# Performance work log

Measured on AMD Instinct MI355X. Metric: run time of the kernel, lower is better.

The kernel has to match this reference:

```python
import jax, jax.numpy as jnp
import numpy as np

N, E, DEG, DIM, NFP, NSEQ = 8192, 65536, 16, 64, 10000, 1024
LGNN, RAD, LOUT, NCLS = 3, 2, 2, 2


def setup_inputs() -> dict:
    key = jax.random.key(0)
    ks = jax.random.split(key, 24)
    s = 0.02
    return {
        "fingerprints": jax.random.randint(ks[0], (N,), 0, NFP + 1),
        "atom_degree_list": jax.random.randint(ks[1], (N, DEG), 0, N),
        "bond_feature": jax.random.normal(ks[2], (E, 10), jnp.float32),
        "bond_degree_list": jax.random.randint(ks[3], (N, DEG), 0, E),
        "i_bond_j": jax.random.randint(ks[4], (E, 2), 0, N),
        # scale down so adjacency @ hs does not saturate the sigmoids
        "adjacency": jax.random.uniform(ks[5], (N, N), jnp.float32) * (1.0 / 128.0),
        "words": jax.random.normal(ks[6], (NSEQ,), jnp.float32),
        "embed_table": jax.random.normal(ks[7], (NFP + 1, DIM), jnp.float32) * s,
        "bond_W": jax.random.normal(ks[8], (10, DIM), jnp.float32) * s,
        "bond_b": jnp.zeros((DIM,), jnp.float32),
        "sub_W": jax.random.normal(ks[9], (RAD, DIM, DIM), jnp.float32) * s,
        "sub_b": jnp.zeros((RAD, DIM), jnp.float32),
        "neigh_W": jax.random.normal(ks[10], (LGNN, 2 * DIM, DIM), jnp.float32) * s,
        "neigh_b": jnp.zeros((LGNN, DIM), jnp.float32),
        "side_W": jax.random.normal(ks[11], (LGNN, DIM, DIM), jnp.float32) * s,
        "side_b": jnp.zeros((LGNN, DIM), jnp.float32),
        "fc_W": jax.random.uniform(ks[12], (NSEQ, DIM), jnp.float32, -0.01, 0.01),
        "fc_b": jnp.zeros((DIM,), jnp.float32),
        "out_W": jax.random.normal(ks[13], (LOUT, 2 * DIM, 2 * DIM), jnp.float32) * s,
        "out_b": jnp.zeros((LOUT, 2 * DIM), jnp.float32),
        "inter_W": jax.random.normal(ks[14], (2 * DIM, NCLS), jnp.float32) * s,
        "inter_b": jnp.zeros((NCLS,), jnp.float32),
    }


def reference(fingerprints, atom_degree_list, bond_feature, bond_degree_list,
              i_bond_j, adjacency, words, embed_table, bond_W, bond_b,
              sub_W, sub_b, neigh_W, neigh_b, side_W, side_b,
              fc_W, fc_b, out_W, out_b, inter_W, inter_b):
    # sub_graph: residual dense-adjacency propagation
    x = embed_table[fingerprints]                       # [N, dim]
    for i in range(RAD):
        hs = jax.nn.relu(x @ sub_W[i] + sub_b[i])
        x = x + adjacency @ hs

    # gnn: gather neighbors, concat, linear+leaky_relu, sum, sigmoid updates
    bond_f = bond_feature @ bond_W + bond_b             # [E, dim]
    atom_f = x
    for i in range(LGNN):
        bn = bond_f[bond_degree_list]                   # [N, DEG, dim]
        an = atom_f[atom_degree_list]                   # [N, DEG, dim]
        nf = jnp.concatenate([an, bn], axis=-1)         # [N, DEG, 2*dim]
        nf = jax.nn.leaky_relu(nf @ neigh_W[i] + neigh_b[i], 0.01)
        atom_f = jax.nn.sigmoid(atom_f + nf.sum(axis=-2))
        pair = atom_f[i_bond_j].sum(axis=-2)            # [E, dim]
        bond_f = jax.nn.sigmoid(bond_f + pair @ side_W[i] + side_b[i])

    disease_vector = jnp.mean(x + atom_f, axis=0)[None, :]   # [1, dim]

    # miRNA vector via MLP
    mirna_vector = words.reshape(1, -1) @ fc_W + fc_b        # [1, dim]

    cat = jnp.concatenate([disease_vector, mirna_vector], axis=1)  # [1, 2*dim]
    for j in range(LOUT):
        cat = jax.nn.relu(cat @ out_W[j] + out_b[j])
    association = cat @ inter_W + inter_b                    # [1, n_classes]
    return association
```

## Files before the change

### kernel.cpp

```cpp
#include <hip/hip_runtime.h>
#include <hip/hip_bf16.h>
#include <cstdint>
#include <cstddef>

#define N_ATOM 8192
#define N_EDGE 65536
#define DEG    16
#define DIM    64
#define ADJ_S  4
#define BM     64
#define BK     64

typedef __attribute__((ext_vector_type(8))) short bf16x8_t;
typedef __attribute__((ext_vector_type(4))) float f32x4_t;

__device__ __forceinline__ float sigmoidf_(float z) {
  return 1.0f / (1.0f + __expf(-z));
}
__device__ __forceinline__ float lrelu_(float z) {
  return z > 0.0f ? z : 0.01f * z;
}
__device__ __forceinline__ unsigned short f2bfu(float f) {
  union { __hip_bfloat16 h; unsigned short u; } v;
  v.h = __float2bfloat16(f);
  return v.u;
}
__device__ __forceinline__ float bf2f(unsigned short u) {
  union { unsigned int i; float f; } v;
  v.i = ((unsigned int)u) << 16;
  return v.f;
}
__device__ __forceinline__ float4 cvt4f(ushort4 u) {
  return make_float4(bf2f(u.x), bf2f(u.y), bf2f(u.z), bf2f(u.w));
}
__device__ __forceinline__ ushort4 cvt4b(float4 f) {
  ushort4 u;
  u.x = f2bfu(f.x); u.y = f2bfu(f.y); u.z = f2bfu(f.z); u.w = f2bfu(f.w);
  return u;
}
__device__ __forceinline__ bf16x8_t cvt8(const float4 a, const float4 b) {
  bf16x8_t r;
  r[0] = (short)f2bfu(a.x); r[1] = (short)f2bfu(a.y);
  r[2] = (short)f2bfu(a.z); r[3] = (short)f2bfu(a.w);
  r[4] = (short)f2bfu(b.x); r[5] = (short)f2bfu(b.y);
  r[6] = (short)f2bfu(b.z); r[7] = (short)f2bfu(b.w);
  return r;
}
__device__ __forceinline__ void gload16(const void* g, void* l) {
  __builtin_amdgcn_global_load_lds(
      (const __attribute__((address_space(1))) void*)g,
      (__attribute__((address_space(3))) void*)l, 16, 0, 0);
}

__global__ __launch_bounds__(256) void k_front(
    const int* __restrict__ fp, const float* __restrict__ emb,
    float* __restrict__ x, const float* __restrict__ W,
    const float* __restrict__ b, unsigned short* __restrict__ hsT,
    const float* __restrict__ bfeat, const float* __restrict__ bW,
    const float* __restrict__ bb, unsigned short* __restrict__ bond_bf,
    const float* __restrict__ Wbn0, unsigned short* __restrict__ B_bf,
    const float* __restrict__ words, const float* __restrict__ fcW,
    float* __restrict__ mp2) {
  __shared__ float ps[64][68];
  __shared__ float Ws[64][64];
  const int t = threadIdx.x;
  const int r = t >> 4, dq = t & 15, d0 = dq * 4;
  if (blockIdx.x < (N_ATOM / 16)) {
    const int row = blockIdx.x * 16 + r;
    float4 v = reinterpret_cast<const float4*>(emb)[(size_t)fp[row] * 16 + dq];
    reinterpret_cast<float4*>(x)[(size_t)row * 16 + dq] = v;
    *reinterpret_cast<float4*>(&ps[r][d0]) = v;
#pragma unroll
    for (int q = 0; q < 4; ++q) {
      int p = t + q * 256;
      reinterpret_cast<float4*>(&Ws[0][0])[p] =
          reinterpret_cast<const float4*>(W)[p];
    }
    __syncthreads();
    float4 acc = reinterpret_cast<const float4*>(b)[dq];
#pragma unroll
    for (int k = 0; k < 64; ++k) {
      float xv = ps[r][k];
      float4 wv = *reinterpret_cast<const float4*>(&Ws[k][d0]);
      acc.x = fmaf(xv, wv.x, acc.x);
      acc.y = fmaf(xv, wv.y, acc.y);
      acc.z = fmaf(xv, wv.z, acc.z);
      acc.w = fmaf(xv, wv.w, acc.w);
    }
    float a4[4] = {acc.x, acc.y, acc.z, acc.w};
#pragma unroll
    for (int j = 0; j < 4; ++j)
      hsT[(size_t)(d0 + j) * N_ATOM + row] = f2bfu(fmaxf(a4[j], 0.0f));
  } else if (blockIdx.x < (N_ATOM / 16 + N_EDGE / 64)) {
    const int row0 = (blockIdx.x - N_ATOM / 16) * 64;
    float4 acc[4];
#pragma unroll
    for (int g = 0; g < 4; ++g) acc[g] = reinterpret_cast<const float4*>(bb)[dq];
#pragma unroll
    for (int k = 0; k < 10; ++k) {
      float4 wv = reinterpret_cast<const float4*>(bW)[k * 16 + dq];
#pragma unroll
      for (int g = 0; g < 4; ++g) {
        float xv = bfeat[(size_t)(row0 + g * 16 + r) * 10 + k];
        acc[g].x = fmaf(xv, wv.x, acc[g].x);
        acc[g].y = fmaf(xv, wv.y, acc[g].y);
        acc[g].z = fmaf(xv, wv.z, acc[g].z);
        acc[g].w = fmaf(xv, wv.w, acc[g].w);
      }
    }
#pragma unroll
    for (int g = 0; g < 4; ++g) {
      int row = row0 + g * 16 + r;
      reinterpret_cast<ushort4*>(bond_bf)[(size_t)row * 16 + dq] = cvt4b(acc[g]);
      *reinterpret_cast<float4*>(&ps[g * 16 + r][d0]) = acc[g];
    }
#pragma unroll
    for (int q = 0; q < 4; ++q) {
      int p = t + q * 256;
      reinterpret_cast<float4*>(&Ws[0][0])[p] =
          reinterpret_cast<const float4*>(Wbn0)[p];
    }
    __syncthreads();
    float4 a2[4];
#pragma unroll
    for (int g = 0; g < 4; ++g) a2[g] = make_float4(0.f, 0.f, 0.f, 0.f);
    for (int k = 0; k < 64; ++k) {
      float4 wv = *reinterpret_cast<const float4*>(&Ws[k][d0]);
#pragma unroll
      for (int g = 0; g < 4; ++g) {
        float xv = ps[g * 16 + r][k];
        a2[g].x = fmaf(xv, wv.x, a2[g].x);
        a2[g].y = fmaf(xv, wv.y, a2[g].y);
        a2[g].z = fmaf(xv, wv.z, a2[g].z);
        a2[g].w = fmaf(xv, wv.w, a2[g].w);
      }
    }
#pragma unroll
    for (int g = 0; g < 4; ++g) {
      int row = row0 + g * 16 + r;
      reinterpret_cast<ushort4*>(B_bf)[(size_t)row * 16 + dq] = cvt4b(a2[g]);
    }
  } else {
    const int mb = blockIdx.x - (N_ATOM / 16 + N_EDGE / 64);
    const int k = mb * 16 + r;
    float wv = words[k];
    float4 fv = reinterpret_cast<const float4*>(fcW)[(size_t)k * 16 + dq];
    float4 acc = make_float4(wv * fv.x, wv * fv.y, wv * fv.z, wv * fv.w);
    float4* red4 = reinterpret_cast<float4*>(&Ws[0][0]);
    red4[t] = acc;
    __syncthreads();
    for (int h = 8; h >= 1; h >>= 1) {
      if (r < h) {
        float4 o = red4[t + h * 16];
        acc.x += o.x; acc.y += o.y; acc.z += o.z; acc.w += o.w;
        red4[t] = acc;
      }
      __syncthreads();
    }
    if (r == 0) reinterpret_cast<float4*>(mp2)[mb * 16 + dq] = acc;
  }
}

__global__ __launch_bounds__(256) void k_red_hs(
    const float* __restrict__ part, float* __restrict__ x,
    const float* __restrict__ W, const float* __restrict__ b,
    unsigned short* __restrict__ hsT) {
  __shared__ float xs[16][68];
  __shared__ float Ws[64][64];
  const int t = threadIdx.x;
  const int r = t >> 4, dq = t & 15, d0 = dq * 4;
  const int row = blockIdx.x * 16 + r;
  float4 v = reinterpret_cast<const float4*>(x)[(size_t)row * 16 + dq];
#pragma unroll
  for (int s = 0; s < ADJ_S; ++s) {
    float4 p = reinterpret_cast<const float4*>(part)
                   [(size_t)s * (N_ATOM * 16) + (size_t)row * 16 + dq];
    v.x += p.x; v.y += p.y; v.z += p.z; v.w += p.w;
  }
  reinterpret_cast<float4*>(x)[(size_t)row * 16 + dq] = v;
  *reinterpret_cast<float4*>(&xs[r][d0]) = v;
#pragma unroll
  for (int q = 0; q < 4; ++q) {
    int p = t + q * 256;
    reinterpret_cast<float4*>(&Ws[0][0])[p] =
        reinterpret_cast<const float4*>(W)[p];
  }
  __syncthreads();
  float4 acc = reinterpret_cast<const float4*>(b)[dq];
#pragma unroll
  for (int k = 0; k < 64; ++k) {
    float xv = xs[r][k];
    float4 wv = *reinterpret_cast<const float4*>(&Ws[k][d0]);
    acc.x = fmaf(xv, wv.x, acc.x);
    acc.y = fmaf(xv, wv.y, acc.y);
    acc.z = fmaf(xv, wv.z, acc.z);
    acc.w = fmaf(xv, wv.w, acc.w);
  }
  float a4[4] = {acc.x, acc.y, acc.z, acc.w};
#pragma unroll
  for (int j = 0; j < 4; ++j)
    hsT[(size_t)(d0 + j) * N_ATOM + row] = f2bfu(fmaxf(a4[j], 0.0f));
}

__global__ __launch_bounds__(256) void k_adjmm(
    const float* __restrict__ adj, const unsigned short* __restrict__ hsT,
    float* __restrict__ part) {
  __shared__ float          Abuf[2][BM * BK];
  __shared__ unsigned short Bbuf[2][64 * BK];
  const int t = threadIdx.x;
  const int lane = t & 63, w = t >> 6;
  const int lr = lane & 15, lg = lane >> 4;
  const int row0 = blockIdx.x * BM;
  const int kbase = blockIdx.y * (N_ATOM / ADJ_S);
  const int NSTEP = (N_ATOM / ADJ_S) / BK;

  size_t aSrc[4]; int aLds[4];
#pragma unroll
  for (int j = 0; j < 4; ++j) {
    int c = j * 256 + t;
    int row = c >> 4, u = c & 15;
    int us = (u & 8) | ((u & 7) ^ (row & 7));
    aSrc[j] = (size_t)(row0 + row) * N_ATOM + kbase + us * 4;
    aLds[j] = j * 1024 + w * 256;
  }
  size_t bSrc[2]; int bLds[2];
#pragma unroll
  for (int j = 0; j < 2; ++j) {
    int c = j * 256 + t;
    int row = c >> 3, u = c & 7;
    int us = u ^ (row & 7);
    bSrc[j] = (size_t)row * N_ATOM + kbase + us * 8;
    bLds[j] = j * 2048 + w * 512;
  }

  f32x4_t acc[4];
#pragma unroll
  for (int n = 0; n < 4; ++n) acc[n] = (f32x4_t){0.f, 0.f, 0.f, 0.f};

#define STAGE(buf, kt)                                                        \
  {                                                                           \
    _Pragma("unroll")                                                         \
    for (int j = 0; j < 4; ++j)                                               \
      gload16(adj + aSrc[j] + (kt) * BK, &Abuf[buf][aLds[j]]);                \
    _Pragma("unroll")                                                         \
    for (int j = 0; j < 2; ++j)                                               \
      gload16(hsT + bSrc[j] + (kt) * BK, &Bbuf[buf][bLds[j]]);                \
  }

  STAGE(0, 0);
  int cur = 0;
  const int Rl = w * 16 + lr;
  for (int kt = 0; kt < NSTEP; ++kt) {
    if (kt + 1 < NSTEP) {
      STAGE(cur ^ 1, kt + 1);
      asm volatile("s_waitcnt vmcnt(6)" ::: "memory");
    } else {
      asm volatile("s_waitcnt vmcnt(0)" ::: "memory");
    }
    __builtin_amdgcn_s_barrier();
    __builtin_amdgcn_sched_barrier(0);
#pragma unroll
    for (int kf = 0; kf < 2; ++kf) {
      int ua = kf * 8 + ((2 * lg) ^ (Rl & 7));
      int ub = kf * 8 + ((2 * lg + 1) ^ (Rl & 7));
      float4 fa = *reinterpret_cast<const float4*>(&Abuf[cur][Rl * 64 + ua * 4]);
      float4 fb = *reinterpret_cast<const float4*>(&Abuf[cur][Rl * 64 + ub * 4]);
      bf16x8_t a = cvt8(fa, fb);
#pragma unroll
      for (int n = 0; n < 4; ++n) {
        int Rb = n * 16 + lr;
        int us = (kf * 4 + lg) ^ (Rb & 7);
        bf16x8_t bv = *reinterpret_cast<const bf16x8_t*>(&Bbuf[cur][Rb * 64 + us * 8]);
        acc[n] = __builtin_amdgcn_mfma_f32_16x16x32_bf16(a, bv, acc[n], 0, 0, 0);
      }
    }
    __builtin_amdgcn_sched_barrier(0);
    __builtin_amdgcn_s_barrier();
    cur ^= 1;
  }
#undef STAGE

  float* pp = part + (size_t)blockIdx.y * (N_ATOM * DIM);
#pragma unroll
  for (int n = 0; n < 4; ++n)
#pragma unroll
    for (int rg = 0; rg < 4; ++rg) {
      int row = row0 + w * 16 + lg * 4 + rg;
      int col = n * 16 + lr;
      pp[(size_t)row * DIM + col] = acc[n][rg];
    }
}

__global__ __launch_bounds__(256) void k_A0(
    float* __restrict__ atom_f, const float* __restrict__ nW0,
    const float* __restrict__ nb0, unsigned short* __restrict__ A,
    const float* __restrict__ part, float* __restrict__ x) {
  __shared__ float xs[16][68];
  __shared__ float Ws[64][64];
  int t = threadIdx.x;
  int r = t >> 4, dq = t & 15, d0 = dq * 4;
  int row = blockIdx.x * 16 + r;
  float4 v = reinterpret_cast<const float4*>(x)[(size_t)row * 16 + dq];
#pragma unroll
  for (int s = 0; s < ADJ_S; ++s) {
    float4 p = reinterpret_cast<const float4*>(part)
                   [(size_t)s * (N_ATOM * 16) + (size_t)row * 16 + dq];
    v.x += p.x; v.y += p.y; v.z += p.z; v.w += p.w;
  }
  reinterpret_cast<float4*>(x)[(size_t)row * 16 + dq] = v;
  reinterpret_cast<float4*>(atom_f)[(size_t)row * 16 + dq] = v;
  *reinterpret_cast<float4*>(&xs[r][d0]) = v;
#pragma unroll
  for (int q = 0; q < 4; ++q) {
    int p = t + q * 256;
    reinterpret_cast<float4*>(&Ws[0][0])[p] = reinterpret_cast<const float4*>(nW0)[p];
  }
  __syncthreads();
  float4 acc = reinterpret_cast<const float4*>(nb0)[dq];
#pragma unroll
  for (int k = 0; k < 64; ++k) {
    float xv = xs[r][k];
    float4 wv = *reinterpret_cast<const float4*>(&Ws[k][d0]);
    acc.x = fmaf(xv, wv.x, acc.x);
    acc.y = fmaf(xv, wv.y, acc.y);
    acc.z = fmaf(xv, wv.z, acc.z);
    acc.w = fmaf(xv, wv.w, acc.w);
  }
  reinterpret_cast<ushort4*>(A)[(size_t)row * 16 + dq] = cvt4b(acc);
}

__global__ __launch_bounds__(256) void k_upd(
    const int* __restrict__ adl, const int* __restrict__ bdl,
    const unsigned short* __restrict__ A, const unsigned short* __restrict__ B,
    float* __restrict__ atom_f, const float* __restrict__ WanN,
    const float* __restrict__ nbN, unsigned short* __restrict__ A_next,
    const float* __restrict__ x, float* __restrict__ mp, int has_next) {
  __shared__ float xs[16][68];
  __shared__ float Ws[64][64];
  int t = threadIdx.x;
  int r = t >> 4, dq = t & 15, d0 = dq * 4;
  int n = blockIdx.x * 16 + r;
  float4 s = make_float4(0.f, 0.f, 0.f, 0.f);
#pragma unroll
  for (int g = 0; g < DEG; ++g) {
    int ai = adl[n * DEG + g];
    int bi = bdl[n * DEG + g];
    float4 va = cvt4f(reinterpret_cast<const ushort4*>(A)[(size_t)ai * 16 + dq]);
    float4 vb = cvt4f(reinterpret_cast<const ushort4*>(B)[(size_t)bi * 16 + dq]);
    s.x += lrelu_(va.x + vb.x);
    s.y += lrelu_(va.y + vb.y);
    s.z += lrelu_(va.z + vb.z);
    s.w += lrelu_(va.w + vb.w);
  }
  float4 af = reinterpret_cast<const float4*>(atom_f)[(size_t)n * 16 + dq];
  af.x = sigmoidf_(af.x + s.x);
  af.y = sigmoidf_(af.y + s.y);
  af.z = sigmoidf_(af.z + s.z);
  af.w = sigmoidf_(af.w + s.w);
  reinterpret_cast<float4*>(atom_f)[(size_t)n * 16 + dq] = af;
  if (has_next) {
    *reinterpret_cast<float4*>(&xs[r][d0]) = af;
#pragma unroll
    for (int q = 0; q < 4; ++q) {
      int p = t + q * 256;
      reinterpret_cast<float4*>(&Ws[0][0])[p] =
          reinterpret_cast<const float4*>(WanN)[p];
    }
    __syncthreads();
    float4 acc = reinterpret_cast<const float4*>(nbN)[dq];
#pragma unroll
    for (int k = 0; k < 64; ++k) {
      float xv = xs[r][k];
      float4 wv = *reinterpret_cast<const float4*>(&Ws[k][d0]);
      acc.x = fmaf(xv, wv.x, acc.x);
      acc.y = fmaf(xv, wv.y, acc.y);
      acc.z = fmaf(xv, wv.z, acc.z);
      acc.w = fmaf(xv, wv.w, acc.w);
    }
    reinterpret_cast<ushort4*>(A_next)[(size_t)n * 16 + dq] = cvt4b(acc);
  } else {
    float4 xv = reinterpret_cast<const float4*>(x)[(size_t)n * 16 + dq];
    float4 c = make_float4(af.x + xv.x, af.y + xv.y, af.z + xv.z, af.w + xv.w);
    float4* red4 = reinterpret_cast<float4*>(&Ws[0][0]);
    red4[t] = c;
    __syncthreads();
    for (int h = 8; h >= 1; h >>= 1) {
      if (r < h) {
        float4 o = red4[t + h * 16];
        c.x += o.x; c.y += o.y; c.z += o.z; c.w += o.w;
        red4[t] = c;
      }
      __syncthreads();
    }
    if (r == 0) reinterpret_cast<float4*>(mp)[blockIdx.x * 16 + dq] = c;
  }
}

__global__ __launch_bounds__(256) void k_side(
    const int* __restrict__ ibj, const float* __restrict__ atom_f,
    const float* __restrict__ sW, const float* __restrict__ sb,
    unsigned short* __restrict__ bond_bf, const float* __restrict__ WbnN,
    unsigned short* __restrict__ B_next, int write_bond) {
  __shared__ float ps[64][68];
  __shared__ float Ws[64][64];
  int t = threadIdx.x;
  int r = t >> 4, dq = t & 15, d0 = dq * 4;
  int e0 = blockIdx.x * 64;
#pragma unroll
  for (int q = 0; q < 4; ++q) {
    int p = t + q * 256;
    reinterpret_cast<float4*>(&Ws[0][0])[p] = reinterpret_cast<const float4*>(sW)[p];
  }
#pragma unroll
  for (int g = 0; g < 4; ++g) {
    int e = e0 + g * 16 + r;
    int i0 = ibj[e * 2], i1 = ibj[e * 2 + 1];
    float4 p0 = reinterpret_cast<const float4*>(atom_f)[(size_t)i0 * 16 + dq];
    float4 p1 = reinterpret_cast<const float4*>(atom_f)[(size_t)i1 * 16 + dq];
    *reinterpret_cast<float4*>(&ps[g * 16 + r][d0]) =
        make_float4(p0.x + p1.x, p0.y + p1.y, p0.z + p1.z, p0.w + p1.w);
  }
  __syncthreads();
  float4 acc[4];
#pragma unroll
  for (int g = 0; g < 4; ++g) acc[g] = reinterpret_cast<const float4*>(sb)[dq];
  for (int k = 0; k < 64; ++k) {
    float4 wv = *reinterpret_cast<const float4*>(&Ws[k][d0]);
#pragma unroll
    for (int g = 0; g < 4; ++g) {
      float xv = ps[g * 16 + r][k];
      acc[g].x = fmaf(xv, wv.x, acc[g].x);
      acc[g].y = fmaf(xv, wv.y, acc[g].y);
      acc[g].z = fmaf(xv, wv.z, acc[g].z);
      acc[g].w = fmaf(xv, wv.w, acc[g].w);
    }
  }
  float4 bf[4];
#pragma unroll
  for (int g = 0; g < 4; ++g) {
    int e = e0 + g * 16 + r;
    float4 b0 = cvt4f(reinterpret_cast<const ushort4*>(bond_bf)[(size_t)e * 16 + dq]);
    bf[g].x = sigmoidf_(b0.x + acc[g].x);
    bf[g].y = sigmoidf_(b0.y + acc[g].y);
    bf[g].z = sigmoidf_(b0.z + acc[g].z);
    bf[g].w = sigmoidf_(b0.w + acc[g].w);
    if (write_bond)
      reinterpret_cast<ushort4*>(bond_bf)[(size_t)e * 16 + dq] = cvt4b(bf[g]);
  }
  __syncthreads();
#pragma unroll
  for (int g = 0; g < 4; ++g)
    *reinterpret_cast<float4*>(&ps[g * 16 + r][d0]) = bf[g];
#pragma unroll
  for (int q = 0; q < 4; ++q) {
    int p = t + q * 256;
    reinterpret_cast<float4*>(&Ws[0][0])[p] =
        reinterpret_cast<const float4*>(WbnN)[p];
  }
  __syncthreads();
  float4 a2[4];
#pragma unroll
  for (int g = 0; g < 4; ++g) a2[g] = make_float4(0.f, 0.f, 0.f, 0.f);
  for (int k = 0; k < 64; ++k) {
    float4 wv = *reinterpret_cast<const float4*>(&Ws[k][d0]);
#pragma unroll
    for (int g = 0; g < 4; ++g) {
      float xv = ps[g * 16 + r][k];
      a2[g].x = fmaf(xv, wv.x, a2[g].x);
      a2[g].y = fmaf(xv, wv.y, a2[g].y);
      a2[g].z = fmaf(xv, wv.z, a2[g].z);
      a2[g].w = fmaf(xv, wv.w, a2[g].w);
    }
  }
#pragma unroll
  for (int g = 0; g < 4; ++g) {
    int e = e0 + g * 16 + r;
    reinterpret_cast<ushort4*>(B_next)[(size_t)e * 16 + dq] = cvt4b(a2[g]);
  }
}

__global__ __launch_bounds__(256) void k_tail(
    const float* __restrict__ mp, const float* __restrict__ mp2,
    const float* __restrict__ fcb, const float* __restrict__ oW,
    const float* __restrict__ ob, const float* __restrict__ iW,
    const float* __restrict__ ib, float* __restrict__ out) {
  __shared__ float red[4][64];
  __shared__ float red2[4][64];
  __shared__ float cat[128];
  int t = threadIdx.x;
  int col = t & 63, ch = t >> 6;
  {
    float s = 0.f;
    for (int w = ch * 128; w < ch * 128 + 128; ++w) s += mp[w * 64 + col];
    red[ch][col] = s;
    float s2 = 0.f;
    for (int w = ch * 16; w < ch * 16 + 16; ++w) s2 += mp2[w * 64 + col];
    red2[ch][col] = s2;
  }
  __syncthreads();
  if (t < 64) {
    cat[t] = (red[0][t] + red[1][t] + red[2][t] + red[3][t]) * (1.0f / N_ATOM);
  } else if (t < 128) {
    int d = t - 64;
    cat[64 + d] = fcb[d] + red2[0][d] + red2[1][d] + red2[2][d] + red2[3][d];
  }
  __syncthreads();
  for (int j = 0; j < 2; ++j) {
    float s = 0.f;
    if (t < 128) {
      s = ob[j * 128 + t];
      for (int k = 0; k < 128; ++k)
        s = fmaf(cat[k], oW[(size_t)j * 128 * 128 + k * 128 + t], s);
      s = fmaxf(s, 0.f);
    }
    __syncthreads();
    if (t < 128) cat[t] = s;
    __syncthreads();
  }
  if (t < 2) {
    float s = ib[t];
    for (int k = 0; k < 128; ++k) s = fmaf(cat[k], iW[k * 2 + t], s);
    out[t] = s;
  }
}

extern "C" void kernel_launch(void* const* d_in, const int* in_sizes, int n_in,
                              void* d_out, int out_size, void* d_ws, size_t ws_size,
                              hipStream_t stream) {
  const int*   fp    = (const int*)  d_in[0];
  const int*   adl   = (const int*)  d_in[1];
  const float* bfeat = (const float*)d_in[2];
  const int*   bdl   = (const int*)  d_in[3];
  const int*   ibj   = (const int*)  d_in[4];
  const float* adj   = (const float*)d_in[5];
  const float* words = (const float*)d_in[6];
  const float* emb   = (const float*)d_in[7];
  const float* bW    = (const float*)d_in[8];
  const float* bb    = (const float*)d_in[9];
  const float* subW  = (const float*)d_in[10];
  const float* subb  = (const float*)d_in[11];
  const float* nW    = (const float*)d_in[12];
  const float* nb    = (const float*)d_in[13];
  const float* sW    = (const float*)d_in[14];
  const float* sb    = (const float*)d_in[15];
  const float* fcW   = (const float*)d_in[16];
  const float* fcb   = (const float*)d_in[17];
  const float* oW    = (const float*)d_in[18];
  const float* ob    = (const float*)d_in[19];
  const float* iW    = (const float*)d_in[20];
  const float* ib    = (const float*)d_in[21];
  float* out = (float*)d_out;

  char* ws = (char*)d_ws;
  const size_t MB = 1ull << 20;
  float*          x      = (float*)(ws + 0 * MB);
  float*          atom_f = (float*)(ws + 2 * MB);
  unsigned short* A0_bf  = (unsigned short*)(ws + 4 * MB);
  unsigned short* A1_bf  = (unsigned short*)(ws + 5 * MB);
  unsigned short* hsT    = (unsigned short*)(ws + 6 * MB);
  float*          mp     = (float*)(ws + 7 * MB);
  float*          mp2    = (float*)(ws + 7 * MB + 512 * 1024);
  unsigned short* bond_bf= (unsigned short*)(ws + 8 * MB);
  unsigned short* B_bf   = (unsigned short*)(ws + 16 * MB);
  float*          part   = (float*)(ws + 32 * MB);

  dim3 gmm(N_ATOM / BM, ADJ_S);

  k_front<<<N_ATOM / 16 + N_EDGE / 64 + 64, 256, 0, stream>>>(
      fp, emb, x, subW, subb, hsT, bfeat, bW, bb, bond_bf,
      nW + 64 * 64, B_bf, words, fcW, mp2);
  k_adjmm<<<gmm, 256, 0, stream>>>(adj, hsT, part);
  k_red_hs<<<N_ATOM / 16, 256, 0, stream>>>(part, x, subW + 64 * 64,
                                            subb + 64, hsT);
  k_adjmm<<<gmm, 256, 0, stream>>>(adj, hsT, part);

  k_A0<<<N_ATOM / 16, 256, 0, stream>>>(atom_f, nW, nb, A0_bf, part, x);
  k_upd<<<N_ATOM / 16, 256, 0, stream>>>(adl, bdl, A0_bf, B_bf, atom_f,
                                         nW + 1 * 128 * 64, nb + 1 * 64,
                                         A1_bf, x, mp, 1);
  k_side<<<N_EDGE / 64, 256, 0, stream>>>(ibj, atom_f, sW, sb, bond_bf,
                                          nW + 1 * 128 * 64 + 64 * 64, B_bf, 1);
  k_upd<<<N_ATOM / 16, 256, 0, stream>>>(adl, bdl, A1_bf, B_bf, atom_f,
                                         nW + 2 * 128 * 64, nb + 2 * 64,
                                         A0_bf, x, mp, 1);
  k_side<<<N_EDGE / 64, 256, 0, stream>>>(ibj, atom_f, sW + 64 * 64, sb + 64,
                                          bond_bf, nW + 2 * 128 * 64 + 64 * 64,
                                          B_bf, 0);
  k_upd<<<N_ATOM / 16, 256, 0, stream>>>(adl, bdl, A0_bf, B_bf, atom_f,
                                         nullptr, nullptr, nullptr, x, mp, 0);

  k_tail<<<1, 256, 0, stream>>>(mp, mp2, fcb, oW, ob, iW, ib, out);
}
```

Before: 218.0 us.

## Fuse adjacency matmul with reduction and dense epilogue, dropping split-K partials

Replaces the split-K adjacency GEMM (64-row tiles, 4 K-splits writing fp32 partials) and its separate reduce/dense kernels with one kernel per radius step. Each block owns 16 rows and covers the full K range with triple-buffered loads, then applies the residual add and the next 64x64 dense layer in its epilogue. This removes the partial-sum traffic and two launches. In exchange each block reads the whole hsT for only 16 rows, which cuts B reuse fourfold, and the grid becomes 512 blocks with long serial K loops.

```diff
diff --git a/kernel.cpp b/kernel.cpp
--- a/kernel.cpp
+++ b/kernel.cpp
@@ -7,8 +7,6 @@
 #define N_EDGE 65536
 #define DEG    16
 #define DIM    64
-#define ADJ_S  4
-#define BM     64
 #define BK     64
 
 typedef __attribute__((ext_vector_type(8))) short bf16x8_t;
@@ -161,99 +159,54 @@
   }
 }
 
-__global__ __launch_bounds__(256) void k_red_hs(
-    const float* __restrict__ part, float* __restrict__ x,
-    const float* __restrict__ W, const float* __restrict__ b,
-    unsigned short* __restrict__ hsT) {
-  __shared__ float xs[16][68];
-  __shared__ float Ws[64][64];
-  const int t = threadIdx.x;
-  const int r = t >> 4, dq = t & 15, d0 = dq * 4;
-  const int row = blockIdx.x * 16 + r;
-  float4 v = reinterpret_cast<const float4*>(x)[(size_t)row * 16 + dq];
-#pragma unroll
-  for (int s = 0; s < ADJ_S; ++s) {
-    float4 p = reinterpret_cast<const float4*>(part)
-                   [(size_t)s * (N_ATOM * 16) + (size_t)row * 16 + dq];
-    v.x += p.x; v.y += p.y; v.z += p.z; v.w += p.w;
-  }
-  reinterpret_cast<float4*>(x)[(size_t)row * 16 + dq] = v;
-  *reinterpret_cast<float4*>(&xs[r][d0]) = v;
-#pragma unroll
-  for (int q = 0; q < 4; ++q) {
-    int p = t + q * 256;
-    reinterpret_cast<float4*>(&Ws[0][0])[p] =
-        reinterpret_cast<const float4*>(W)[p];
-  }
-  __syncthreads();
-  float4 acc = reinterpret_cast<const float4*>(b)[dq];
-#pragma unroll
-  for (int k = 0; k < 64; ++k) {
-    float xv = xs[r][k];
-    float4 wv = *reinterpret_cast<const float4*>(&Ws[k][d0]);
-    acc.x = fmaf(xv, wv.x, acc.x);
-    acc.y = fmaf(xv, wv.y, acc.y);
-    acc.z = fmaf(xv, wv.z, acc.z);
-    acc.w = fmaf(xv, wv.w, acc.w);
-  }
-  float a4[4] = {acc.x, acc.y, acc.z, acc.w};
-#pragma unroll
-  for (int j = 0; j < 4; ++j)
-    hsT[(size_t)(d0 + j) * N_ATOM + row] = f2bfu(fmaxf(a4[j], 0.0f));
-}
-
-__global__ __launch_bounds__(256) void k_adjmm(
-    const float* __restrict__ adj, const unsigned short* __restrict__ hsT,
-    float* __restrict__ part) {
-  __shared__ float          Abuf[2][BM * BK];
-  __shared__ unsigned short Bbuf[2][64 * BK];
+__global__ __launch_bounds__(256) void k_adjfused(
+    const float* __restrict__ adj, const unsigned short* __restrict__ hsIn,
+    float* __restrict__ x, float* __restrict__ atom_f,
+    const float* __restrict__ Wn, const float* __restrict__ bn,
+    unsigned short* __restrict__ hsOut, unsigned short* __restrict__ A0,
+    int mode) {
+  __shared__ float          Abuf[3][16 * BK];
+  __shared__ unsigned short Bbuf[3][64 * BK];
   const int t = threadIdx.x;
   const int lane = t & 63, w = t >> 6;
   const int lr = lane & 15, lg = lane >> 4;
-  const int row0 = blockIdx.x * BM;
-  const int kbase = blockIdx.y * (N_ATOM / ADJ_S);
-  const int NSTEP = (N_ATOM / ADJ_S) / BK;
-
-  size_t aSrc[4]; int aLds[4];
-#pragma unroll
-  for (int j = 0; j < 4; ++j) {
-    int c = j * 256 + t;
-    int row = c >> 4, u = c & 15;
-    int us = (u & 8) | ((u & 7) ^ (row & 7));
-    aSrc[j] = (size_t)(row0 + row) * N_ATOM + kbase + us * 4;
-    aLds[j] = j * 1024 + w * 256;
-  }
+  const int row0 = blockIdx.x * 16;
+  const int NSTEP = N_ATOM / BK;
+
+  const int arow = t >> 4, au = t & 15;
+  const int aus = (au & 8) | ((au & 7) ^ (arow & 7));
+  const size_t aSrc = (size_t)(row0 + arow) * N_ATOM + aus * 4;
+  const int aLds = w * 256;
   size_t bSrc[2]; int bLds[2];
 #pragma unroll
   for (int j = 0; j < 2; ++j) {
     int c = j * 256 + t;
-    int row = c >> 3, u = c & 7;
-    int us = u ^ (row & 7);
-    bSrc[j] = (size_t)row * N_ATOM + kbase + us * 8;
+    int brow = c >> 3, bu = c & 7;
+    int bus = bu ^ (brow & 7);
+    bSrc[j] = (size_t)brow * N_ATOM + bus * 8;
     bLds[j] = j * 2048 + w * 512;
   }
 
-  f32x4_t acc[4];
-#pragma unroll
-  for (int n = 0; n < 4; ++n) acc[n] = (f32x4_t){0.f, 0.f, 0.f, 0.f};
+  f32x4_t acc = (f32x4_t){0.f, 0.f, 0.f, 0.f};
 
 #define STAGE(buf, kt)                                                        \
   {                                                                           \
-    _Pragma("unroll")                                                         \
-    for (int j = 0; j < 4; ++j)                                               \
-      gload16(adj + aSrc[j] + (kt) * BK, &Abuf[buf][aLds[j]]);                \
+    gload16(adj + aSrc + (size_t)(kt) * BK, &Abuf[buf][aLds]);                \
     _Pragma("unroll")                                                         \
     for (int j = 0; j < 2; ++j)                                               \
-      gload16(hsT + bSrc[j] + (kt) * BK, &Bbuf[buf][bLds[j]]);                \
+      gload16(hsIn + bSrc[j] + (size_t)(kt) * BK, &Bbuf[buf][bLds[j]]);       \
   }
 
   STAGE(0, 0);
+  STAGE(1, 1);
   int cur = 0;
-  const int Rl = w * 16 + lr;
   for (int kt = 0; kt < NSTEP; ++kt) {
-    if (kt + 1 < NSTEP) {
-      STAGE(cur ^ 1, kt + 1);
+    if (kt + 2 < NSTEP) {
+      int nb = cur + 2; if (nb >= 3) nb -= 3;
+      STAGE(nb, kt + 2);
       asm volatile("s_waitcnt vmcnt(6)" ::: "memory");
+    } else if (kt + 1 < NSTEP) {
+      asm volatile("s_waitcnt vmcnt(3)" ::: "memory");
     } else {
       asm volatile("s_waitcnt vmcnt(0)" ::: "memory");
     }
@@ -261,72 +214,65 @@
     __builtin_amdgcn_sched_barrier(0);
 #pragma unroll
     for (int kf = 0; kf < 2; ++kf) {
-      int ua = kf * 8 + ((2 * lg) ^ (Rl & 7));
-      int ub = kf * 8 + ((2 * lg + 1) ^ (Rl & 7));
-      float4 fa = *reinterpret_cast<const float4*>(&Abuf[cur][Rl * 64 + ua * 4]);
-      float4 fb = *reinterpret_cast<const float4*>(&Abuf[cur][Rl * 64 + ub * 4]);
+      int ua = kf * 8 + ((2 * lg) ^ (lr & 7));
+      int ub = kf * 8 + ((2 * lg + 1) ^ (lr & 7));
+      float4 fa = *reinterpret_cast<const float4*>(&Abuf[cur][lr * 64 + ua * 4]);
+      float4 fb = *reinterpret_cast<const float4*>(&Abuf[cur][lr * 64 + ub * 4]);
       bf16x8_t a = cvt8(fa, fb);
-#pragma unroll
-      for (int n = 0; n < 4; ++n) {
-        int Rb = n * 16 + lr;
-        int us = (kf * 4 + lg) ^ (Rb & 7);
-        bf16x8_t bv = *reinterpret_cast<const bf16x8_t*>(&Bbuf[cur][Rb * 64 + us * 8]);
-        acc[n] = __builtin_amdgcn_mfma_f32_16x16x32_bf16(a, bv, acc[n], 0, 0, 0);
-      }
+      int Rb = w * 16 + lr;
+      int us = (kf * 4 + lg) ^ (Rb & 7);
+      bf16x8_t bv = *reinterpret_cast<const bf16x8_t*>(&Bbuf[cur][Rb * 64 + us * 8]);
+      acc = __builtin_amdgcn_mfma_f32_16x16x32_bf16(a, bv, acc, 0, 0, 0);
     }
     __builtin_amdgcn_sched_barrier(0);
     __builtin_amdgcn_s_barrier();
-    cur ^= 1;
+    cur = cur + 1; if (cur >= 3) cur = 0;
   }
 #undef STAGE
 
-  float* pp = part + (size_t)blockIdx.y * (N_ATOM * DIM);
-#pragma unroll
-  for (int n = 0; n < 4; ++n)
-#pragma unroll
-    for (int rg = 0; rg < 4; ++rg) {
-      int row = row0 + w * 16 + lg * 4 + rg;
-      int col = n * 16 + lr;
-      pp[(size_t)row * DIM + col] = acc[n][rg];
-    }
-}
-
-__global__ __launch_bounds__(256) void k_A0(
-    float* __restrict__ atom_f, const float* __restrict__ nW0,
-    const float* __restrict__ nb0, unsigned short* __restrict__ A,
-    const float* __restrict__ part, float* __restrict__ x) {
-  __shared__ float xs[16][68];
-  __shared__ float Ws[64][64];
-  int t = threadIdx.x;
-  int r = t >> 4, dq = t & 15, d0 = dq * 4;
-  int row = blockIdx.x * 16 + r;
-  float4 v = reinterpret_cast<const float4*>(x)[(size_t)row * 16 + dq];
-#pragma unroll
-  for (int s = 0; s < ADJ_S; ++s) {
-    float4 p = reinterpret_cast<const float4*>(part)
-                   [(size_t)s * (N_ATOM * 16) + (size_t)row * 16 + dq];
-    v.x += p.x; v.y += p.y; v.z += p.z; v.w += p.w;
-  }
-  reinterpret_cast<float4*>(x)[(size_t)row * 16 + dq] = v;
-  reinterpret_cast<float4*>(atom_f)[(size_t)row * 16 + dq] = v;
-  *reinterpret_cast<float4*>(&xs[r][d0]) = v;
+  float* xs  = &Abuf[0][0];
+  float* Wsh = reinterpret_cast<float*>(&Bbuf[0][0]);
+#pragma unroll
+  for (int rg = 0; rg < 4; ++rg)
+    xs[(lg * 4 + rg) * 68 + w * 16 + lr] = acc[rg];
 #pragma unroll
   for (int q = 0; q < 4; ++q) {
     int p = t + q * 256;
-    reinterpret_cast<float4*>(&Ws[0][0])[p] = reinterpret_cast<const float4*>(nW0)[p];
-  }
-  __syncthreads();
-  float4 acc = reinterpret_cast<const float4*>(nb0)[dq];
+    reinterpret_cast<float4*>(Wsh)[p] = reinterpret_cast<const float4*>(Wn)[p];
+  }
+  __syncthreads();
+  const int r = t >> 4, dq = t & 15, d0 = dq * 4;
+  const int row = row0 + r;
+  float4 xv = reinterpret_cast<const float4*>(x)[(size_t)row * 16 + dq];
+  float4 v = make_float4(xv.x + xs[r * 68 + d0 + 0],
+                         xv.y + xs[r * 68 + d0 + 1],
+                         xv.z + xs[r * 68 + d0 + 2],
+                         xv.w + xs[r * 68 + d0 + 3]);
+  reinterpret_cast<float4*>(x)[(size_t)row * 16 + dq] = v;
+  if (mode) reinterpret_cast<float4*>(atom_f)[(size_t)row * 16 + dq] = v;
+  xs[r * 68 + d0 + 0] = v.x;
+  xs[r * 68 + d0 + 1] = v.y;
+  xs[r * 68 + d0 + 2] = v.z;
+  xs[r * 68 + d0 + 3] = v.w;
+  __syncthreads();
+  float4 acc2 = reinterpret_cast<const float4*>(bn)[dq];
 #pragma unroll
   for (int k = 0; k < 64; ++k) {
-    float xv = xs[r][k];
-    float4 wv = *reinterpret_cast<const float4*>(&Ws[k][d0]);
-    acc.x = fmaf(xv, wv.x, acc.x);
-    acc.y = fmaf(xv, wv.y, acc.y);
-    acc.z = fmaf(xv, wv.z, acc.z);
-    acc.w = fmaf(xv, wv.w, acc.w);
-  }
-  reinterpret_cast<ushort4*>(A)[(size_t)row * 16 + dq] = cvt4b(acc);
+    float xk = xs[r * 68 + k];
+    float4 wv = *reinterpret_cast<const float4*>(&Wsh[k * 64 + d0]);
+    acc2.x = fmaf(xk, wv.x, acc2.x);
+    acc2.y = fmaf(xk, wv.y, acc2.y);
+    acc2.z = fmaf(xk, wv.z, acc2.z);
+    acc2.w = fmaf(xk, wv.w, acc2.w);
+  }
+  if (mode == 0) {
+    float a4[4] = {acc2.x, acc2.y, acc2.z, acc2.w};
+#pragma unroll
+    for (int j = 0; j < 4; ++j)
+      hsOut[(size_t)(d0 + j) * N_ATOM + row] = f2bfu(fmaxf(a4[j], 0.0f));
+  } else {
+    reinterpret_cast<ushort4*>(A0)[(size_t)row * 16 + dq] = cvt4b(acc2);
+  }
 }
 
 __global__ __launch_bounds__(256) void k_upd(
@@ -557,24 +503,21 @@
   float*          atom_f = (float*)(ws + 2 * MB);
   unsigned short* A0_bf  = (unsigned short*)(ws + 4 * MB);
   unsigned short* A1_bf  = (unsigned short*)(ws + 5 * MB);
-  unsigned short* hsT    = (unsigned short*)(ws + 6 * MB);
-  float*          mp     = (float*)(ws + 7 * MB);
-  float*          mp2    = (float*)(ws + 7 * MB + 512 * 1024);
+  unsigned short* hsT_a  = (unsigned short*)(ws + 6 * MB);
+  unsigned short* hsT_b  = (unsigned short*)(ws + 7 * MB);
   unsigned short* bond_bf= (unsigned short*)(ws + 8 * MB);
   unsigned short* B_bf   = (unsigned short*)(ws + 16 * MB);
-  float*          part   = (float*)(ws + 32 * MB);
-
-  dim3 gmm(N_ATOM / BM, ADJ_S);
+  float*          mp     = (float*)(ws + 24 * MB);
+  float*          mp2    = (float*)(ws + 25 * MB);
 
   k_front<<<N_ATOM / 16 + N_EDGE / 64 + 64, 256, 0, stream>>>(
-      fp, emb, x, subW, subb, hsT, bfeat, bW, bb, bond_bf,
+      fp, emb, x, subW, subb, hsT_a, bfeat, bW, bb, bond_bf,
       nW + 64 * 64, B_bf, words, fcW, mp2);
-  k_adjmm<<<gmm, 256, 0, stream>>>(adj, hsT, part);
-  k_red_hs<<<N_ATOM / 16, 256, 0, stream>>>(part, x, subW + 64 * 64,
-                                            subb + 64, hsT);
-  k_adjmm<<<gmm, 256, 0, stream>>>(adj, hsT, part);
-
-  k_A0<<<N_ATOM / 16, 256, 0, stream>>>(atom_f, nW, nb, A0_bf, part, x);
+  k_adjfused<<<N_ATOM / 16, 256, 0, stream>>>(
+      adj, hsT_a, x, atom_f, subW + 64 * 64, subb + 64, hsT_b, A0_bf, 0);
+  k_adjfused<<<N_ATOM / 16, 256, 0, stream>>>(
+      adj, hsT_b, x, atom_f, nW, nb, hsT_a, A0_bf, 1);
+
   k_upd<<<N_ATOM / 16, 256, 0, stream>>>(adl, bdl, A0_bf, B_bf, atom_f,
                                          nW + 1 * 128 * 64, nb + 1 * 64,
                                          A1_bf, x, mp, 1);
```

New measurement: 310.9 us. 42.6% more time.
